# Kernel tuning notes

Hardware: AMD Instinct MI355X
Metric: run time of the kernel (lower is better)

## Reference

```python
import jax, jax.numpy as jnp
import numpy as np

N, E, D, H, L, QD = 100000, 640000, 128, 256, 3, 768


def setup_inputs() -> dict:
    key = jax.random.key(0)
    ks = jax.random.split(key, 16)
    def W(k, shape, fan):
        return jax.random.normal(k, shape, jnp.float32) / np.float32(np.sqrt(fan))
    return {
        "node_embedding": jax.random.normal(ks[0], (N, D), jnp.float32),
        "relation_embedding": jax.random.normal(ks[1], (E, D), jnp.float32),
        "question_embedding": jax.random.normal(ks[2], (1, QD), jnp.float32),
        "edge_index": jax.random.randint(ks[3], (2, E), 0, N),
        "edge_type": jax.random.randint(ks[4], (E,), 0, 2000),
        "qW": W(ks[5], (QD, D), QD),
        "qb": jnp.zeros((D,), jnp.float32),
        "eW1": W(ks[6], (L, 4 * D, H), 4 * D),
        "eb1": jnp.zeros((L, H), jnp.float32),
        "eW2": W(ks[7], (L, H, D), H),
        "eb2": jnp.zeros((L, D), jnp.float32),
        "nW1": W(ks[8], (L, 2 * D, H), 2 * D),
        "nb1": jnp.zeros((L, H), jnp.float32),
        "nW2": W(ks[9], (L, H, D), H),
        "nb2": jnp.zeros((L, D), jnp.float32),
        "esW": W(ks[10], (D, 1), D),
        "esb": jnp.zeros((1,), jnp.float32),
        "nsW": W(ks[11], (D, 1), D),
        "nsb": jnp.zeros((1,), jnp.float32),
    }


def reference(node_embedding, relation_embedding, question_embedding, edge_index,
              edge_type, qW, qb, eW1, eb1, eW2, eb2, nW1, nb1, nW2, nb2,
              esW, esb, nsW, nsb):
    # edge_type is unused in the original forward as well.
    q = question_embedding @ qW + qb  # [1, D]
    src, dst = edge_index[0], edge_index[1]
    node_h = node_embedding  # [N, D]
    edge_h = relation_embedding  # [E, D]
    num_layers = eW1.shape[0]
    for l in range(num_layers):
        edge_src = node_h[src]  # gather [E, D]
        edge_dst = node_h[dst]  # gather [E, D]
        q_exp = jnp.broadcast_to(q, (edge_src.shape[0], q.shape[1]))
        edge_feat = jnp.concatenate([edge_src, edge_dst, edge_h, q_exp], axis=-1)  # [E, 4D]
        h = jax.nn.relu(edge_feat @ eW1[l] + eb1[l])
        edge_h = h @ eW2[l] + eb2[l]  # [E, D]
        # scatter-add to both endpoints (index_add_ on src then dst)
        agg = jnp.zeros_like(node_h).at[src].add(edge_h).at[dst].add(edge_h)
        nh = jax.nn.relu(jnp.concatenate([node_h, agg], axis=-1) @ nW1[l] + nb1[l])
        node_h = nh @ nW2[l] + nb2[l]
    edge_scores = jax.nn.sigmoid((edge_h @ esW + esb).squeeze(-1))  # [E]
    node_scores = jax.nn.sigmoid((node_h @ nsW + nsb).squeeze(-1))  # [N]
    return node_scores, edge_scores
```

## Files before the change

kernel.cpp:

```cpp
#include <hip/hip_runtime.h>
#include <math.h>

#define NN 100000
#define NE 640000
#define DD 128
#define HH 256
#define NL 3
#define QDIM 768
#define TM 64

#define A1P 392
#define A2P 264

typedef _Float16 h16x8 __attribute__((ext_vector_type(8)));
typedef float f32x4 __attribute__((ext_vector_type(4)));

#define MFMA16(A, B, C) __builtin_amdgcn_mfma_f32_16x16x32_f16(A, B, C, 0, 0, 0)

__device__ __forceinline__ unsigned short f2h_bits(float f) {
    _Float16 h = (_Float16)f;
    return __builtin_bit_cast(unsigned short, h);
}

__global__ void q_kernel(const float* __restrict__ qe, const float* __restrict__ qW,
                         const float* __restrict__ qb, float* __restrict__ q) {
    int d = threadIdx.x;
    float acc = qb[d];
    for (int k = 0; k < QDIM; ++k) acc = fmaf(qe[k], qW[k * DD + d], acc);
    q[d] = acc;
}

__global__ void qc_kernel(const float* __restrict__ q, const float* __restrict__ eW1,
                          const float* __restrict__ eb1, float* __restrict__ qc) {
    int l = blockIdx.x;
    int h = threadIdx.x;
    const float* W = eW1 + ((size_t)l * 4 * DD + 3 * DD) * HH;
    __shared__ float sq[DD];
    if (h < DD) sq[h] = q[h];
    __syncthreads();
    float acc = eb1[l * HH + h];
    for (int d = 0; d < DD; ++d) acc = fmaf(sq[d], W[d * HH + h], acc);
    qc[l * HH + h] = acc;
}

__global__ void pack_kernel(const float* __restrict__ W, unsigned short* __restrict__ out,
                            int K, int Ncols, int lstride, size_t plane ) {
    int nct = Ncols >> 4;
    int bx = blockIdx.x;
    int l = blockIdx.y;
    int lane = threadIdx.x;
    const float* Wl = W + (size_t)l * lstride;
    int kt = bx / nct, ct = bx - kt * nct;
    int r = kt * 32 + (lane >> 4) * 8;
    int c = ct * 16 + (lane & 15);
    unsigned vh[4], vl[4];
#pragma unroll
    for (int p = 0; p < 4; ++p) {
        float x0 = Wl[(size_t)(r + 2 * p) * Ncols + c];
        float x1 = Wl[(size_t)(r + 2 * p + 1) * Ncols + c];
        _Float16 h0 = (_Float16)x0, h1 = (_Float16)x1;
        _Float16 l0 = (_Float16)(x0 - (float)h0), l1 = (_Float16)(x1 - (float)h1);
        vh[p] = (unsigned)__builtin_bit_cast(unsigned short, h0) |
                ((unsigned)__builtin_bit_cast(unsigned short, h1) << 16);
        vl[p] = (unsigned)__builtin_bit_cast(unsigned short, l0) |
                ((unsigned)__builtin_bit_cast(unsigned short, l1) << 16);
    }
    size_t off = (size_t)l * K * Ncols + ((size_t)bx * 64 + lane) * 8;
    *(uint4*)(out + off) = make_uint4(vh[0], vh[1], vh[2], vh[3]);
    *(uint4*)(out + plane + off) = make_uint4(vl[0], vl[1], vl[2], vl[3]);
}

__global__ void deg_kernel(const int* __restrict__ eidx, int* __restrict__ cnt) {
    int i = blockIdx.x * 256 + threadIdx.x;
    if (i < 2 * NE) atomicAdd(&cnt[eidx[i]], 1);
}

#define SCAN_T 1024
__global__ void scan_kernel(const int* __restrict__ cnt, int* __restrict__ offsets,
                            int* __restrict__ cursor) {
    __shared__ int s[SCAN_T];
    int t = threadIdx.x;
    const int chunk = (NN + SCAN_T - 1) / SCAN_T;
    int lo = t * chunk, hi = lo + chunk; if (hi > NN) hi = NN;
    int sum = 0;
    for (int i = lo; i < hi; ++i) sum += cnt[i];
    s[t] = sum;
    __syncthreads();
    for (int off = 1; off < SCAN_T; off <<= 1) {
        int v = (t >= off) ? s[t - off] : 0;
        __syncthreads();
        s[t] += v;
        __syncthreads();
    }
    int run = (t == 0) ? 0 : s[t - 1];
    for (int i = lo; i < hi; ++i) {
        int c = cnt[i];
        offsets[i] = run;
        cursor[i] = run;
        run += c;
    }
    if (t == SCAN_T - 1) offsets[NN] = run;
}

__global__ void fill_kernel(const int* __restrict__ eidx, int* __restrict__ cursor,
                            int* __restrict__ inc) {
    int i = blockIdx.x * 256 + threadIdx.x;
    if (i < 2 * NE) {
        int e = (i < NE) ? i : i - NE;
        int pos = atomicAdd(&cursor[eidx[i]], 1);
        inc[pos] = e;
    }
}

__global__ __launch_bounds__(256, 3) void edge_kernel(
    const float* __restrict__ node_h, float* __restrict__ edge_h,
    const int* __restrict__ eidx,
    const unsigned short* __restrict__ W1hi, const unsigned short* __restrict__ W1lo,
    const float* __restrict__ qc,
    const unsigned short* __restrict__ W2hi, const unsigned short* __restrict__ W2lo,
    const float* __restrict__ b2)
{
    __shared__ unsigned short sA[TM * A1P];
    unsigned short* sA1 = sA;
    unsigned short* sA2 = sA;

    const int tid = threadIdx.x;
    const int e0 = blockIdx.x * TM;

    const int row = tid >> 2, t4 = tid & 3;
    const int srcn = eidx[e0 + row];
    const int dstn = eidx[NE + e0 + row];

    {
        const float* b0 = node_h + (size_t)srcn * DD;
        const float* b1 = node_h + (size_t)dstn * DD;
        const float* b2p = edge_h + (size_t)(e0 + row) * DD;
#pragma unroll
        for (int i = 0; i < 24; ++i) {
            int seg = i >> 3;
            int k = (t4 + 4 * i) * 4;
            int klocal = k - seg * DD;
            const float* g = (seg == 0) ? b0 : (seg == 1) ? b1 : b2p;
            float4 v = *(const float4*)(g + klocal);
            uint2 p;
            p.x = (unsigned)f2h_bits(v.x) | ((unsigned)f2h_bits(v.y) << 16);
            p.y = (unsigned)f2h_bits(v.z) | ((unsigned)f2h_bits(v.w) << 16);
            *(uint2*)&sA1[row * A1P + k] = p;
        }
    }

    const int lane = tid & 63;
    const int w = tid >> 6;
    const int lrow = lane & 15;
    const int q4 = lane >> 4;

    f32x4 acc[4][4];
#pragma unroll
    for (int ct = 0; ct < 4; ++ct) {
        float iv = qc[w * 64 + ct * 16 + lrow];
        f32x4 c = {iv, iv, iv, iv};
#pragma unroll
        for (int rt = 0; rt < 4; ++rt) acc[rt][ct] = c;
    }
    __syncthreads();

    const h16x8* W1h = (const h16x8*)W1hi;
    const h16x8* W1l = (const h16x8*)W1lo;
    for (int kt = 0; kt < 12; ++kt) {
        h16x8 a[4];
#pragma unroll
        for (int rt = 0; rt < 4; ++rt)
            a[rt] = *(const h16x8*)&sA1[(lrow + 16 * rt) * A1P + kt * 32 + q4 * 8];
#pragma unroll
        for (int ct = 0; ct < 4; ++ct) {
            h16x8 bh = W1h[(kt * 16 + w * 4 + ct) * 64 + lane];
            h16x8 bl = W1l[(kt * 16 + w * 4 + ct) * 64 + lane];
#pragma unroll
            for (int rt = 0; rt < 4; ++rt) {
                acc[rt][ct] = MFMA16(a[rt], bh, acc[rt][ct]);
                acc[rt][ct] = MFMA16(a[rt], bl, acc[rt][ct]);
            }
        }
    }

    __syncthreads();

#pragma unroll
    for (int rt = 0; rt < 4; ++rt)
#pragma unroll
        for (int ct = 0; ct < 4; ++ct)
#pragma unroll
            for (int j = 0; j < 4; ++j) {
                int hr = rt * 16 + q4 * 4 + j;
                int hc = w * 64 + ct * 16 + lrow;
                sA2[hr * A2P + hc] = f2h_bits(fmaxf(acc[rt][ct][j], 0.0f));
            }
    __syncthreads();

    f32x4 acc2[4][2];
#pragma unroll
    for (int ct = 0; ct < 2; ++ct) {
        float iv = b2[w * 32 + ct * 16 + lrow];
        f32x4 c = {iv, iv, iv, iv};
#pragma unroll
        for (int rt = 0; rt < 4; ++rt) acc2[rt][ct] = c;
    }
    const h16x8* W2h = (const h16x8*)W2hi;
    const h16x8* W2l = (const h16x8*)W2lo;
    for (int kt = 0; kt < 8; ++kt) {
        h16x8 a[4];
#pragma unroll
        for (int rt = 0; rt < 4; ++rt)
            a[rt] = *(const h16x8*)&sA2[(lrow + 16 * rt) * A2P + kt * 32 + q4 * 8];
#pragma unroll
        for (int ct = 0; ct < 2; ++ct) {
            h16x8 bh = W2h[(kt * 8 + w * 2 + ct) * 64 + lane];
            h16x8 bl = W2l[(kt * 8 + w * 2 + ct) * 64 + lane];
#pragma unroll
            for (int rt = 0; rt < 4; ++rt) {
                acc2[rt][ct] = MFMA16(a[rt], bh, acc2[rt][ct]);
                acc2[rt][ct] = MFMA16(a[rt], bl, acc2[rt][ct]);
            }
        }
    }

#pragma unroll
    for (int rt = 0; rt < 4; ++rt)
#pragma unroll
        for (int j = 0; j < 4; ++j) {
            int e = e0 + rt * 16 + q4 * 4 + j;
#pragma unroll
            for (int ct = 0; ct < 2; ++ct) {
                int c = w * 32 + ct * 16 + lrow;
                edge_h[(size_t)e * DD + c] = acc2[rt][ct][j];
            }
        }
}

__global__ __launch_bounds__(256, 3) void node_kernel(
    float* __restrict__ node_h, const float* __restrict__ edge_h,
    const int* __restrict__ offsets, const int* __restrict__ inc,
    const unsigned short* __restrict__ W1hi, const unsigned short* __restrict__ W1lo,
    const float* __restrict__ b1,
    const unsigned short* __restrict__ W2hi, const unsigned short* __restrict__ W2lo,
    const float* __restrict__ b2)
{
    __shared__ unsigned short sA[TM * A2P];
    unsigned short* sA1 = sA;
    unsigned short* sA2 = sA;

    const int tid = threadIdx.x;
    const int n0 = blockIdx.x * TM;

    const int row = tid >> 2, t4 = tid & 3;
    const int n = n0 + row;
    const bool vrow = (n < NN);

    if (vrow) {
        const float* g0 = node_h + (size_t)n * DD;
#pragma unroll
        for (int i = 0; i < 8; ++i) {
            int k = (t4 + 4 * i) * 4;
            float4 v = *(const float4*)(g0 + k);
            uint2 p;
            p.x = (unsigned)f2h_bits(v.x) | ((unsigned)f2h_bits(v.y) << 16);
            p.y = (unsigned)f2h_bits(v.z) | ((unsigned)f2h_bits(v.w) << 16);
            *(uint2*)&sA1[row * A2P + k] = p;
        }
    } else {
        uint2 z; z.x = 0; z.y = 0;
#pragma unroll
        for (int i = 0; i < 8; ++i)
            *(uint2*)&sA1[row * A2P + (t4 + 4 * i) * 4] = z;
    }

    {
        int k0 = 0, k1 = 0;
        if (vrow) { k0 = offsets[n]; k1 = offsets[n + 1]; }
        float a[32];
#pragma unroll
        for (int j = 0; j < 32; ++j) a[j] = 0.0f;
        for (int k = k0; k < k1; ++k) {
            int e = inc[k];
            const float* er = edge_h + (size_t)e * DD;
#pragma unroll
            for (int j = 0; j < 8; ++j) {
                float4 v = *(const float4*)(er + j * 16 + t4 * 4);
                a[j * 4 + 0] += v.x;
                a[j * 4 + 1] += v.y;
                a[j * 4 + 2] += v.z;
                a[j * 4 + 3] += v.w;
            }
        }
#pragma unroll
        for (int j = 0; j < 8; ++j) {
            int c = 128 + j * 16 + t4 * 4;
            uint2 p;
            p.x = (unsigned)f2h_bits(a[j * 4 + 0]) | ((unsigned)f2h_bits(a[j * 4 + 1]) << 16);
            p.y = (unsigned)f2h_bits(a[j * 4 + 2]) | ((unsigned)f2h_bits(a[j * 4 + 3]) << 16);
            *(uint2*)&sA1[row * A2P + c] = p;
        }
    }

    const int lane = tid & 63;
    const int w = tid >> 6;
    const int lrow = lane & 15;
    const int q4 = lane >> 4;

    f32x4 acc[4][4];
#pragma unroll
    for (int ct = 0; ct < 4; ++ct) {
        float iv = b1[w * 64 + ct * 16 + lrow];
        f32x4 c = {iv, iv, iv, iv};
#pragma unroll
        for (int rt = 0; rt < 4; ++rt) acc[rt][ct] = c;
    }
    __syncthreads();

    const h16x8* W1h = (const h16x8*)W1hi;
    const h16x8* W1l = (const h16x8*)W1lo;
    for (int kt = 0; kt < 8; ++kt) {
        h16x8 a[4];
#pragma unroll
        for (int rt = 0; rt < 4; ++rt)
            a[rt] = *(const h16x8*)&sA1[(lrow + 16 * rt) * A2P + kt * 32 + q4 * 8];
#pragma unroll
        for (int ct = 0; ct < 4; ++ct) {
            h16x8 bh = W1h[(kt * 16 + w * 4 + ct) * 64 + lane];
            h16x8 bl = W1l[(kt * 16 + w * 4 + ct) * 64 + lane];
#pragma unroll
            for (int rt = 0; rt < 4; ++rt) {
                acc[rt][ct] = MFMA16(a[rt], bh, acc[rt][ct]);
                acc[rt][ct] = MFMA16(a[rt], bl, acc[rt][ct]);
            }
        }
    }

    __syncthreads();

#pragma unroll
    for (int rt = 0; rt < 4; ++rt)
#pragma unroll
        for (int ct = 0; ct < 4; ++ct)
#pragma unroll
            for (int j = 0; j < 4; ++j) {
                int hr = rt * 16 + q4 * 4 + j;
                int hc = w * 64 + ct * 16 + lrow;
                sA2[hr * A2P + hc] = f2h_bits(fmaxf(acc[rt][ct][j], 0.0f));
            }
    __syncthreads();

    f32x4 acc2[4][2];
#pragma unroll
    for (int ct = 0; ct < 2; ++ct) {
        float iv = b2[w * 32 + ct * 16 + lrow];
        f32x4 c = {iv, iv, iv, iv};
#pragma unroll
        for (int rt = 0; rt < 4; ++rt) acc2[rt][ct] = c;
    }
    const h16x8* W2h = (const h16x8*)W2hi;
    const h16x8* W2l = (const h16x8*)W2lo;
    for (int kt = 0; kt < 8; ++kt) {
        h16x8 a[4];
#pragma unroll
        for (int rt = 0; rt < 4; ++rt)
            a[rt] = *(const h16x8*)&sA2[(lrow + 16 * rt) * A2P + kt * 32 + q4 * 8];
#pragma unroll
        for (int ct = 0; ct < 2; ++ct) {
            h16x8 bh = W2h[(kt * 8 + w * 2 + ct) * 64 + lane];
            h16x8 bl = W2l[(kt * 8 + w * 2 + ct) * 64 + lane];
#pragma unroll
            for (int rt = 0; rt < 4; ++rt) {
                acc2[rt][ct] = MFMA16(a[rt], bh, acc2[rt][ct]);
                acc2[rt][ct] = MFMA16(a[rt], bl, acc2[rt][ct]);
            }
        }
    }

#pragma unroll
    for (int rt = 0; rt < 4; ++rt)
#pragma unroll
        for (int j = 0; j < 4; ++j) {
            int rr = rt * 16 + q4 * 4 + j;
            if (n0 + rr < NN) {
#pragma unroll
                for (int ct = 0; ct < 2; ++ct) {
                    int c = w * 32 + ct * 16 + lrow;
                    node_h[(size_t)(n0 + rr) * DD + c] = acc2[rt][ct][j];
                }
            }
        }
}

__global__ void score_kernel(const float* __restrict__ hmat, const float* __restrict__ w,
                             const float* __restrict__ b, float* __restrict__ out) {
    int wid = threadIdx.x >> 6;
    int lane = threadIdx.x & 63;
    int row = blockIdx.x * 4 + wid;
    float2 v  = *(const float2*)(hmat + (size_t)row * DD + lane * 2);
    float2 wv = *(const float2*)(w + lane * 2);
    float s = v.x * wv.x + v.y * wv.y;
#pragma unroll
    for (int off = 32; off; off >>= 1) s += __shfl_down(s, off);
    if (lane == 0) out[row] = 1.0f / (1.0f + expf(-(s + b[0])));
}

extern "C" void kernel_launch(void* const* d_in, const int* in_sizes, int n_in,
                              void* d_out, int out_size, void* d_ws, size_t ws_size,
                              hipStream_t stream) {
    float* node_h = (float*)d_in[0];
    float* edge_h = (float*)d_in[1];
    const float* qe   = (const float*)d_in[2];
    const int*   eidx = (const int*)d_in[3];
    const float* qW  = (const float*)d_in[5];
    const float* qb  = (const float*)d_in[6];
    const float* eW1 = (const float*)d_in[7];
    const float* eb1 = (const float*)d_in[8];
    const float* eW2 = (const float*)d_in[9];
    const float* eb2 = (const float*)d_in[10];
    const float* nW1 = (const float*)d_in[11];
    const float* nb1 = (const float*)d_in[12];
    const float* nW2 = (const float*)d_in[13];
    const float* nb2 = (const float*)d_in[14];
    const float* esW = (const float*)d_in[15];
    const float* esb = (const float*)d_in[16];
    const float* nsW = (const float*)d_in[17];
    const float* nsb = (const float*)d_in[18];

    float* ws  = (float*)d_ws;
    float* q   = ws;
    float* qc  = ws + 256;
    int* cnt     = (int*)(ws + 1024);
    int* cursor  = cnt + NN;
    int* offsets = cursor + NN;
    int* inc     = offsets + NN + 1;

    unsigned short* packs = (unsigned short*)d_out;
    const size_t pe1 = (size_t)NL * 384 * 256;
    const size_t pe2 = (size_t)NL * 256 * 128;
    const size_t pn1 = (size_t)NL * 256 * 256;
    const size_t pn2 = (size_t)NL * 256 * 128;
    unsigned short* eW1p = packs;
    unsigned short* eW2p = eW1p + 2 * pe1;
    unsigned short* nW1p = eW2p + 2 * pe2;
    unsigned short* nW2p = nW1p + 2 * pn1;

    q_kernel<<<1, DD, 0, stream>>>(qe, qW, qb, q);
    qc_kernel<<<NL, HH, 0, stream>>>(q, eW1, eb1, qc);
    pack_kernel<<<dim3(12 * 16, NL), 64, 0, stream>>>(eW1, eW1p, 384, 256, 4 * DD * HH, pe1);
    pack_kernel<<<dim3(8 * 8, NL), 64, 0, stream>>>(eW2, eW2p, 256, 128, HH * DD, pe2);
    pack_kernel<<<dim3(8 * 16, NL), 64, 0, stream>>>(nW1, nW1p, 256, 256, 2 * DD * HH, pn1);
    pack_kernel<<<dim3(8 * 8, NL), 64, 0, stream>>>(nW2, nW2p, 256, 128, HH * DD, pn2);

    hipMemsetAsync(cnt, 0, NN * sizeof(int), stream);
    deg_kernel<<<(2 * NE + 255) / 256, 256, 0, stream>>>(eidx, cnt);
    scan_kernel<<<1, SCAN_T, 0, stream>>>(cnt, offsets, cursor);
    fill_kernel<<<(2 * NE + 255) / 256, 256, 0, stream>>>(eidx, cursor, inc);

    for (int l = 0; l < NL; ++l) {
        edge_kernel<<<NE / TM, 256, 0, stream>>>(
            node_h, edge_h, eidx,
            eW1p + (size_t)l * 384 * 256, eW1p + pe1 + (size_t)l * 384 * 256,
            qc + l * HH,
            eW2p + (size_t)l * 256 * 128, eW2p + pe2 + (size_t)l * 256 * 128,
            eb2 + l * DD);
        node_kernel<<<(NN + TM - 1) / TM, 256, 0, stream>>>(
            node_h, edge_h, offsets, inc,
            nW1p + (size_t)l * 256 * 256, nW1p + pn1 + (size_t)l * 256 * 256,
            nb1 + l * HH,
            nW2p + (size_t)l * 256 * 128, nW2p + pn2 + (size_t)l * 256 * 128,
            nb2 + l * DD);
    }

    score_kernel<<<NN / 4, 256, 0, stream>>>(node_h, nsW, nsb, (float*)d_out);
    score_kernel<<<NE / 4, 256, 0, stream>>>(edge_h, esW, esb, (float*)d_out + NN);
}
```

Baseline: 2.664 ms.

## Store intermediate node and edge features as fp16 with LDS-staged coalesced writes

After layer 0, node and edge hidden states are written as fp16 into the existing buffers, keeping the 512-byte row stride. Later layers' edge gathers, the node scatter-sum reads and the score kernels then read half the bytes per row. Outputs are first staged through shared memory, so each thread writes contiguous 16-byte chunks instead of scattered 4-byte stores. The cost is fp16 rounding of stored activations, including the per-edge values summed during aggregation, plus extra barriers and template variants for the fp32 first layer.

After: 2.302 ms. 1.16x faster.

```diff
diff --git a/kernel.cpp b/kernel.cpp
--- a/kernel.cpp
+++ b/kernel.cpp
@@ -11,6 +11,7 @@
 
 #define A1P 392
 #define A2P 264
+#define OP  136
 
 typedef _Float16 h16x8 __attribute__((ext_vector_type(8)));
 typedef float f32x4 __attribute__((ext_vector_type(4)));
@@ -20,6 +21,12 @@
 __device__ __forceinline__ unsigned short f2h_bits(float f) {
     _Float16 h = (_Float16)f;
     return __builtin_bit_cast(unsigned short, h);
+}
+__device__ __forceinline__ unsigned pk2(float a, float b) {
+    return (unsigned)f2h_bits(a) | ((unsigned)f2h_bits(b) << 16);
+}
+__device__ __forceinline__ float h2f(unsigned short u) {
+    return (float)__builtin_bit_cast(_Float16, u);
 }
 
 __global__ void q_kernel(const float* __restrict__ qe, const float* __restrict__ qW,
@@ -112,8 +119,10 @@
     }
 }
 
+template <bool IN16>
 __global__ __launch_bounds__(256, 3) void edge_kernel(
-    const float* __restrict__ node_h, float* __restrict__ edge_h,
+    const void* node_in, const void* edge_in,
+    unsigned short* edge_out,
     const int* __restrict__ eidx,
     const unsigned short* __restrict__ W1hi, const unsigned short* __restrict__ W1lo,
     const float* __restrict__ qc,
@@ -123,6 +132,7 @@
     __shared__ unsigned short sA[TM * A1P];
     unsigned short* sA1 = sA;
     unsigned short* sA2 = sA;
+    unsigned short* sOut = sA;
 
     const int tid = threadIdx.x;
     const int e0 = blockIdx.x * TM;
@@ -131,21 +141,31 @@
     const int srcn = eidx[e0 + row];
     const int dstn = eidx[NE + e0 + row];
 
-    {
-        const float* b0 = node_h + (size_t)srcn * DD;
-        const float* b1 = node_h + (size_t)dstn * DD;
-        const float* b2p = edge_h + (size_t)(e0 + row) * DD;
-#pragma unroll
-        for (int i = 0; i < 24; ++i) {
-            int seg = i >> 3;
-            int k = (t4 + 4 * i) * 4;
-            int klocal = k - seg * DD;
-            const float* g = (seg == 0) ? b0 : (seg == 1) ? b1 : b2p;
-            float4 v = *(const float4*)(g + klocal);
-            uint2 p;
-            p.x = (unsigned)f2h_bits(v.x) | ((unsigned)f2h_bits(v.y) << 16);
-            p.y = (unsigned)f2h_bits(v.z) | ((unsigned)f2h_bits(v.w) << 16);
-            *(uint2*)&sA1[row * A1P + k] = p;
+    if (IN16) {
+        const unsigned short* b0 = (const unsigned short*)node_in + (size_t)srcn * 256;
+        const unsigned short* b1 = (const unsigned short*)node_in + (size_t)dstn * 256;
+        const unsigned short* bp = (const unsigned short*)edge_in + (size_t)(e0 + row) * 256;
+#pragma unroll
+        for (int i = 0; i < 12; ++i) {
+            int seg = i >> 2, j = i & 3;
+            int c = (t4 + 4 * j) * 8;
+            const unsigned short* g = (seg == 0) ? b0 : (seg == 1) ? b1 : bp;
+            *(uint4*)&sA1[row * A1P + seg * 128 + c] = *(const uint4*)(g + c);
+        }
+    } else {
+        const float* b0 = (const float*)node_in + (size_t)srcn * DD;
+        const float* b1 = (const float*)node_in + (size_t)dstn * DD;
+        const float* bp = (const float*)edge_in + (size_t)(e0 + row) * DD;
+#pragma unroll
+        for (int i = 0; i < 12; ++i) {
+            int seg = i >> 2, j = i & 3;
+            int c = (t4 + 4 * j) * 8;
+            const float* g = (seg == 0) ? b0 : (seg == 1) ? b1 : bp;
+            float4 v0 = *(const float4*)(g + c);
+            float4 v1 = *(const float4*)(g + c + 4);
+            uint4 p = make_uint4(pk2(v0.x, v0.y), pk2(v0.z, v0.w),
+                                 pk2(v1.x, v1.y), pk2(v1.z, v1.w));
+            *(uint4*)&sA1[row * A1P + seg * 128 + c] = p;
         }
     }
 
@@ -224,21 +244,29 @@
         }
     }
 
+    __syncthreads();
 #pragma unroll
     for (int rt = 0; rt < 4; ++rt)
 #pragma unroll
         for (int j = 0; j < 4; ++j) {
-            int e = e0 + rt * 16 + q4 * 4 + j;
-#pragma unroll
-            for (int ct = 0; ct < 2; ++ct) {
-                int c = w * 32 + ct * 16 + lrow;
-                edge_h[(size_t)e * DD + c] = acc2[rt][ct][j];
-            }
-        }
-}
-
+            int rr = rt * 16 + q4 * 4 + j;
+#pragma unroll
+            for (int ct = 0; ct < 2; ++ct)
+                sOut[rr * OP + w * 32 + ct * 16 + lrow] = f2h_bits(acc2[rt][ct][j]);
+        }
+    __syncthreads();
+    {
+        unsigned short* er = edge_out + (size_t)(e0 + row) * 256;
+#pragma unroll
+        for (int j = 0; j < 4; ++j)
+            *(uint4*)(er + t4 * 32 + j * 8) = *(const uint4*)&sOut[row * OP + t4 * 32 + j * 8];
+    }
+}
+
+template <bool IN16>
 __global__ __launch_bounds__(256, 3) void node_kernel(
-    float* __restrict__ node_h, const float* __restrict__ edge_h,
+    const void* node_in, unsigned short* node_out,
+    const unsigned short* __restrict__ edge16,
     const int* __restrict__ offsets, const int* __restrict__ inc,
     const unsigned short* __restrict__ W1hi, const unsigned short* __restrict__ W1lo,
     const float* __restrict__ b1,
@@ -248,6 +276,7 @@
     __shared__ unsigned short sA[TM * A2P];
     unsigned short* sA1 = sA;
     unsigned short* sA2 = sA;
+    unsigned short* sOut = sA;
 
     const int tid = threadIdx.x;
     const int n0 = blockIdx.x * TM;
@@ -257,21 +286,30 @@
     const bool vrow = (n < NN);
 
     if (vrow) {
-        const float* g0 = node_h + (size_t)n * DD;
-#pragma unroll
-        for (int i = 0; i < 8; ++i) {
-            int k = (t4 + 4 * i) * 4;
-            float4 v = *(const float4*)(g0 + k);
-            uint2 p;
-            p.x = (unsigned)f2h_bits(v.x) | ((unsigned)f2h_bits(v.y) << 16);
-            p.y = (unsigned)f2h_bits(v.z) | ((unsigned)f2h_bits(v.w) << 16);
-            *(uint2*)&sA1[row * A2P + k] = p;
+        if (IN16) {
+            const unsigned short* g0 = (const unsigned short*)node_in + (size_t)n * 256;
+#pragma unroll
+            for (int j = 0; j < 4; ++j) {
+                int c = t4 * 32 + j * 8;
+                *(uint4*)&sA1[row * A2P + c] = *(const uint4*)(g0 + c);
+            }
+        } else {
+            const float* g0 = (const float*)node_in + (size_t)n * DD;
+#pragma unroll
+            for (int j = 0; j < 4; ++j) {
+                int c = t4 * 32 + j * 8;
+                float4 v0 = *(const float4*)(g0 + c);
+                float4 v1 = *(const float4*)(g0 + c + 4);
+                uint4 p = make_uint4(pk2(v0.x, v0.y), pk2(v0.z, v0.w),
+                                     pk2(v1.x, v1.y), pk2(v1.z, v1.w));
+                *(uint4*)&sA1[row * A2P + c] = p;
+            }
         }
     } else {
-        uint2 z; z.x = 0; z.y = 0;
-#pragma unroll
-        for (int i = 0; i < 8; ++i)
-            *(uint2*)&sA1[row * A2P + (t4 + 4 * i) * 4] = z;
+        uint4 z = make_uint4(0, 0, 0, 0);
+#pragma unroll
+        for (int j = 0; j < 4; ++j)
+            *(uint4*)&sA1[row * A2P + t4 * 32 + j * 8] = z;
     }
 
     {
@@ -282,23 +320,25 @@
         for (int j = 0; j < 32; ++j) a[j] = 0.0f;
         for (int k = k0; k < k1; ++k) {
             int e = inc[k];
-            const float* er = edge_h + (size_t)e * DD;
-#pragma unroll
-            for (int j = 0; j < 8; ++j) {
-                float4 v = *(const float4*)(er + j * 16 + t4 * 4);
-                a[j * 4 + 0] += v.x;
-                a[j * 4 + 1] += v.y;
-                a[j * 4 + 2] += v.z;
-                a[j * 4 + 3] += v.w;
-            }
-        }
-#pragma unroll
-        for (int j = 0; j < 8; ++j) {
-            int c = 128 + j * 16 + t4 * 4;
-            uint2 p;
-            p.x = (unsigned)f2h_bits(a[j * 4 + 0]) | ((unsigned)f2h_bits(a[j * 4 + 1]) << 16);
-            p.y = (unsigned)f2h_bits(a[j * 4 + 2]) | ((unsigned)f2h_bits(a[j * 4 + 3]) << 16);
-            *(uint2*)&sA1[row * A2P + c] = p;
+            const unsigned short* er = edge16 + (size_t)e * 256 + t4 * 32;
+#pragma unroll
+            for (int j = 0; j < 4; ++j) {
+                uint4 v = *(const uint4*)(er + j * 8);
+                a[j * 8 + 0] += h2f((unsigned short)(v.x & 0xffff));
+                a[j * 8 + 1] += h2f((unsigned short)(v.x >> 16));
+                a[j * 8 + 2] += h2f((unsigned short)(v.y & 0xffff));
+                a[j * 8 + 3] += h2f((unsigned short)(v.y >> 16));
+                a[j * 8 + 4] += h2f((unsigned short)(v.z & 0xffff));
+                a[j * 8 + 5] += h2f((unsigned short)(v.z >> 16));
+                a[j * 8 + 6] += h2f((unsigned short)(v.w & 0xffff));
+                a[j * 8 + 7] += h2f((unsigned short)(v.w >> 16));
+            }
+        }
+#pragma unroll
+        for (int j = 0; j < 4; ++j) {
+            uint4 p = make_uint4(pk2(a[j * 8 + 0], a[j * 8 + 1]), pk2(a[j * 8 + 2], a[j * 8 + 3]),
+                                 pk2(a[j * 8 + 4], a[j * 8 + 5]), pk2(a[j * 8 + 6], a[j * 8 + 7]));
+            *(uint4*)&sA1[row * A2P + 128 + t4 * 32 + j * 8] = p;
         }
     }
 
@@ -377,29 +417,35 @@
         }
     }
 
+    __syncthreads();
 #pragma unroll
     for (int rt = 0; rt < 4; ++rt)
 #pragma unroll
         for (int j = 0; j < 4; ++j) {
             int rr = rt * 16 + q4 * 4 + j;
-            if (n0 + rr < NN) {
-#pragma unroll
-                for (int ct = 0; ct < 2; ++ct) {
-                    int c = w * 32 + ct * 16 + lrow;
-                    node_h[(size_t)(n0 + rr) * DD + c] = acc2[rt][ct][j];
-                }
-            }
-        }
-}
-
-__global__ void score_kernel(const float* __restrict__ hmat, const float* __restrict__ w,
+#pragma unroll
+            for (int ct = 0; ct < 2; ++ct)
+                sOut[rr * OP + w * 32 + ct * 16 + lrow] = f2h_bits(acc2[rt][ct][j]);
+        }
+    __syncthreads();
+    if (vrow) {
+        unsigned short* nr = node_out + (size_t)n * 256;
+#pragma unroll
+        for (int j = 0; j < 4; ++j)
+            *(uint4*)(nr + t4 * 32 + j * 8) = *(const uint4*)&sOut[row * OP + t4 * 32 + j * 8];
+    }
+}
+
+__global__ void score_kernel(const unsigned short* __restrict__ hmat,
+                             const float* __restrict__ w,
                              const float* __restrict__ b, float* __restrict__ out) {
     int wid = threadIdx.x >> 6;
     int lane = threadIdx.x & 63;
     int row = blockIdx.x * 4 + wid;
-    float2 v  = *(const float2*)(hmat + (size_t)row * DD + lane * 2);
+    unsigned v = *(const unsigned*)(hmat + (size_t)row * 256 + lane * 2);
     float2 wv = *(const float2*)(w + lane * 2);
-    float s = v.x * wv.x + v.y * wv.y;
+    float s = h2f((unsigned short)(v & 0xffff)) * wv.x +
+              h2f((unsigned short)(v >> 16)) * wv.y;
 #pragma unroll
     for (int off = 32; off; off >>= 1) s += __shfl_down(s, off);
     if (lane == 0) out[row] = 1.0f / (1.0f + expf(-(s + b[0])));
@@ -427,6 +473,9 @@
     const float* nsW = (const float*)d_in[17];
     const float* nsb = (const float*)d_in[18];
 
+    unsigned short* nh16 = (unsigned short*)node_h;
+    unsigned short* eh16 = (unsigned short*)edge_h;
+
     float* ws  = (float*)d_ws;
     float* q   = ws;
     float* qc  = ws + 256;
@@ -458,20 +507,35 @@
     fill_kernel<<<(2 * NE + 255) / 256, 256, 0, stream>>>(eidx, cursor, inc);
 
     for (int l = 0; l < NL; ++l) {
-        edge_kernel<<<NE / TM, 256, 0, stream>>>(
-            node_h, edge_h, eidx,
-            eW1p + (size_t)l * 384 * 256, eW1p + pe1 + (size_t)l * 384 * 256,
-            qc + l * HH,
-            eW2p + (size_t)l * 256 * 128, eW2p + pe2 + (size_t)l * 256 * 128,
-            eb2 + l * DD);
-        node_kernel<<<(NN + TM - 1) / TM, 256, 0, stream>>>(
-            node_h, edge_h, offsets, inc,
-            nW1p + (size_t)l * 256 * 256, nW1p + pn1 + (size_t)l * 256 * 256,
-            nb1 + l * HH,
-            nW2p + (size_t)l * 256 * 128, nW2p + pn2 + (size_t)l * 256 * 128,
-            nb2 + l * DD);
-    }
-
-    score_kernel<<<NN / 4, 256, 0, stream>>>(node_h, nsW, nsb, (float*)d_out);
-    score_kernel<<<NE / 4, 256, 0, stream>>>(edge_h, esW, esb, (float*)d_out + NN);
-}
+        if (l == 0) {
+            edge_kernel<false><<<NE / TM, 256, 0, stream>>>(
+                (const void*)node_h, (const void*)edge_h, eh16, eidx,
+                eW1p + (size_t)l * 384 * 256, eW1p + pe1 + (size_t)l * 384 * 256,
+                qc + l * HH,
+                eW2p + (size_t)l * 256 * 128, eW2p + pe2 + (size_t)l * 256 * 128,
+                eb2 + l * DD);
+            node_kernel<false><<<(NN + TM - 1) / TM, 256, 0, stream>>>(
+                (const void*)node_h, nh16, eh16, offsets, inc,
+                nW1p + (size_t)l * 256 * 256, nW1p + pn1 + (size_t)l * 256 * 256,
+                nb1 + l * HH,
+                nW2p + (size_t)l * 256 * 128, nW2p + pn2 + (size_t)l * 256 * 128,
+                nb2 + l * DD);
+        } else {
+            edge_kernel<true><<<NE / TM, 256, 0, stream>>>(
+                (const void*)nh16, (const void*)eh16, eh16, eidx,
+                eW1p + (size_t)l * 384 * 256, eW1p + pe1 + (size_t)l * 384 * 256,
+                qc + l * HH,
+                eW2p + (size_t)l * 256 * 128, eW2p + pe2 + (size_t)l * 256 * 128,
+                eb2 + l * DD);
+            node_kernel<true><<<(NN + TM - 1) / TM, 256, 0, stream>>>(
+                (const void*)nh16, nh16, eh16, offsets, inc,
+                nW1p + (size_t)l * 256 * 256, nW1p + pn1 + (size_t)l * 256 * 256,
+                nb1 + l * HH,
+                nW2p + (size_t)l * 256 * 128, nW2p + pn2 + (size_t)l * 256 * 128,
+                nb2 + l * DD);
+        }
+    }
+
+    score_kernel<<<NN / 4, 256, 0, stream>>>(nh16, nsW, nsb, (float*)d_out);
+    score_kernel<<<NE / 4, 256, 0, stream>>>(eh16, esW, esb, (float*)d_out + NN);
+}
```
